# Kernel tuning notes

Measured on AMD Instinct MI355X. Metric: run time of the kernel, lower is better.

## Reference

```python
import jax, jax.numpy as jnp
import numpy as np

H, KVH, DH = 16, 4, 64
DIM = 1024
SCALE_BASE = 4096  # context_len
EPS = 1e-6


def rmsnorm(x, g):
    return x * jax.lax.rsqrt(jnp.mean(x * x, axis=-1, keepdims=True) + EPS) * g


def rope_tables(n, dh, dtype):
    inv_freq = 1.0 / (10000.0 ** (jnp.arange(0, dh, 2, dtype=jnp.float32) / dh))
    t = jnp.arange(n, dtype=jnp.float32) * (SCALE_BASE / n)
    freqs = t[:, None] * inv_freq[None, :]          # [n, dh/2]
    emb = jnp.concatenate([freqs, freqs], axis=-1)  # [n, dh]
    return jnp.cos(emb).astype(dtype), jnp.sin(emb).astype(dtype)


def apply_rope(x, cos, sin):
    # x: [b, h, n, dh]; cos/sin: [n, dh]
    x1, x2 = jnp.split(x, 2, axis=-1)
    rot = jnp.concatenate([-x2, x1], axis=-1)
    return x * cos + rot * sin


def setup_inputs() -> dict:
    key = jax.random.key(0)
    ks = jax.random.split(key, 12)
    B, N = 1, 2048
    std = 0.02
    inp = {
        "x": jax.random.normal(ks[0], (B, N, DIM), jnp.float32),
        "a": jax.random.normal(ks[1], (B, N, DIM), jnp.float32),
        "g_x": jnp.ones((DIM,), jnp.float32),
        "g_a": jnp.ones((DIM,), jnp.float32),
        "Wq_x": jax.random.normal(ks[2], (DIM, H * DH), jnp.float32) * std,
        "Wkv_x": jax.random.normal(ks[3], (DIM, 2 * KVH * DH), jnp.float32) * std,
        "Wq_a": jax.random.normal(ks[4], (DIM, H * DH), jnp.float32) * std,
        "Wkv_a": jax.random.normal(ks[5], (DIM, 2 * KVH * DH), jnp.float32) * std,
        "Wout_x": jax.random.normal(ks[6], (H * DH, DIM), jnp.float32) * std,
        "bout_x": jnp.zeros((DIM,), jnp.float32),
        "Wout_a": jax.random.normal(ks[7], (H * DH, DIM), jnp.float32) * std,
        "bout_a": jnp.zeros((DIM,), jnp.float32),
    }
    return inp


def _split_heads(t, h):
    b, n, hd = t.shape
    return t.reshape(b, n, h, hd // h).transpose(0, 2, 1, 3)  # b h n d


def _stream_qkv(s, g, Wq, Wkv):
    s = rmsnorm(s, g)
    q = _split_heads(s @ Wq, H)                 # [b, H, n, DH]
    kv = s @ Wkv
    k, v = jnp.split(kv, 2, axis=-1)
    k = _split_heads(k, KVH)                    # [b, KVH, n, DH]
    v = _split_heads(v, KVH)
    return q, k, v


def reference(x, a, g_x, g_a, Wq_x, Wkv_x, Wq_a, Wkv_a, Wout_x, bout_x, Wout_a, bout_a):
    B, Nx, _ = x.shape
    Na = a.shape[1]
    scale = DH ** -0.5
    r = H // KVH

    q_x, k_x, v_x = _stream_qkv(x, g_x, Wq_x, Wkv_x)
    q_a, k_a, v_a = _stream_qkv(a, g_a, Wq_a, Wkv_a)

    cos_x, sin_x = rope_tables(Nx, DH, x.dtype)
    cos_a, sin_a = rope_tables(Na, DH, a.dtype)
    q_x, k_x = apply_rope(q_x, cos_x, sin_x), apply_rope(k_x, cos_x, sin_x)
    q_a, k_a = apply_rope(q_a, cos_a, sin_a), apply_rope(k_a, cos_a, sin_a)

    # NOTE: original scales q by dim_head**-0.5 AND sdpa scales again -> 1/DH total
    q_x = q_x * scale
    q_a = q_a * scale

    # GQA expansion: einops 'b h n d -> b (r h) n d' == tile heads
    tile = lambda t: jnp.tile(t, (1, r, 1, 1))
    k_x, v_x, k_a, v_a = tile(k_x), tile(v_x), tile(k_a), tile(v_a)

    # pack [a, x] along seq
    q = jnp.concatenate([q_a, q_x], axis=2)
    k = jnp.concatenate([k_a, k_x], axis=2)
    v = jnp.concatenate([v_a, v_x], axis=2)

    scores = jnp.einsum('bhqd,bhkd->bhqk', q, k) * scale  # sdpa's own scale
    attn = jax.nn.softmax(scores, axis=-1)
    out = jnp.einsum('bhqk,bhkd->bhqd', attn, v)          # [b, H, Na+Nx, DH]

    out_a, out_x = out[:, :, :Na], out[:, :, Na:]
    merge = lambda t: t.transpose(0, 2, 1, 3).reshape(B, -1, H * DH)
    out_x = merge(out_x) @ Wout_x + bout_x
    out_a = merge(out_a) @ Wout_a + bout_a
    return out_x, out_a
```

## Files before the change

### kernel.cpp

```cpp
#include <hip/hip_runtime.h>
#include <hip/hip_bf16.h>
#include <stdint.h>
#include <math.h>


#define NSEQ 2048
#define NJ   4096
#define DIMM 1024
#define LPAD 72

typedef __attribute__((ext_vector_type(4))) float f32x4;
typedef __attribute__((ext_vector_type(8))) short bf16x8;
typedef __attribute__((ext_vector_type(4))) short bf16x4;

__device__ __forceinline__ unsigned short f2bf(float f) {
  union { float f; uint32_t u; } v; v.f = f;
  return (unsigned short)((v.u + 0x7FFFu + ((v.u >> 16) & 1u)) >> 16);
}

__device__ __forceinline__ uint32_t pack2bf(float a, float b) {
  __hip_bfloat162 h = __float22bfloat162_rn(float2{a, b});
  union { __hip_bfloat162 h; uint32_t u; } c; c.h = h;
  return c.u;
}

#if defined(__has_builtin)
#if __has_builtin(__builtin_amdgcn_exp2f)
#define FAST_EXP2(x) __builtin_amdgcn_exp2f(x)
#endif
#endif
#ifndef FAST_EXP2
#define FAST_EXP2(x) exp2f(x)
#endif

__device__ __forceinline__ void glds16(const void* g, void* l) {
  __builtin_amdgcn_global_load_lds(
      (const __attribute__((address_space(1))) unsigned int*)g,
      (__attribute__((address_space(3))) unsigned int*)l, 16, 0, 0);
}

__global__ __launch_bounds__(256) void prep_kernel(
    const float* __restrict__ xa, const float* __restrict__ xx,
    const float* __restrict__ ga, const float* __restrict__ gx,
    const float* __restrict__ wqa, const float* __restrict__ wqx,
    const float* __restrict__ wkva, const float* __restrict__ wkvx,
    const float* __restrict__ woa, const float* __restrict__ wox,
    unsigned short* __restrict__ XN, unsigned short* __restrict__ WQT,
    unsigned short* __restrict__ WKVT, unsigned short* __restrict__ WOT,
    float* __restrict__ cosT, float* __restrict__ sinT) {
  __shared__ float tile[32][33];
  __shared__ float red[4];
  int bid = blockIdx.x, t = threadIdx.x;
  if (bid < 256) {
    int idx = bid * 256 + t;
    int pos = idx >> 5, i = idx & 31;
    double inv = pow(10000.0, -(double)i / 32.0);
    double ang = (double)(2 * pos) * inv;
    cosT[idx] = (float)cos(ang);
    sinT[idx] = (float)sin(ang);
  } else if (bid < 6400) {
    int b = bid - 256;
    int z = b >> 10, yx = b & 1023;
    int n0 = (yx >> 5) * 32, k0 = (yx & 31) * 32;
    int s = z & 1, ty = z >> 1;
    int N = (ty == 1) ? 512 : 1024;
    if (n0 >= N) return;
    const float* src = (z == 0) ? wqa : (z == 1) ? wqx : (z == 2) ? wkva
                     : (z == 3) ? wkvx : (z == 4) ? woa : wox;
    unsigned short* dst = (ty == 0) ? WQT + (size_t)s * 1024 * 1024
                        : (ty == 1) ? WKVT + (size_t)s * 512 * 1024
                                    : WOT + (size_t)s * 1024 * 1024;
    int r = t >> 3, c4 = (t & 7) * 4;
    f32x4 v = *(const f32x4*)(src + (size_t)(k0 + r) * N + n0 + c4);
    tile[r][c4 + 0] = v.x; tile[r][c4 + 1] = v.y;
    tile[r][c4 + 2] = v.z; tile[r][c4 + 3] = v.w;
    __syncthreads();
    int nn = t >> 3, kk = (t & 7) * 4;
    bf16x4 o;
    o.x = (short)f2bf(tile[kk + 0][nn]);
    o.y = (short)f2bf(tile[kk + 1][nn]);
    o.z = (short)f2bf(tile[kk + 2][nn]);
    o.w = (short)f2bf(tile[kk + 3][nn]);
    *(bf16x4*)(dst + (size_t)(n0 + nn) * 1024 + k0 + kk) = o;
  } else {
    int b = bid - 6400;
    int s = b >> 11, row = b & 2047;
    const float* src = (s == 0 ? xa : xx) + (size_t)row * DIMM;
    const float* g = (s == 0 ? ga : gx);
    f32x4 v = *(const f32x4*)(src + t * 4);
    float ss = v.x * v.x + v.y * v.y + v.z * v.z + v.w * v.w;
#pragma unroll
    for (int o = 32; o > 0; o >>= 1) ss += __shfl_xor(ss, o, 64);
    if ((t & 63) == 0) red[t >> 6] = ss;
    __syncthreads();
    float tot = red[0] + red[1] + red[2] + red[3];
    float rs = rsqrtf(tot * (1.0f / DIMM) + 1e-6f);
    f32x4 gv = *(const f32x4*)(g + t * 4);
    bf16x4 o;
    o.x = (short)f2bf(v.x * rs * gv.x);
    o.y = (short)f2bf(v.y * rs * gv.y);
    o.z = (short)f2bf(v.z * rs * gv.z);
    o.w = (short)f2bf(v.w * rs * gv.w);
    *(bf16x4*)(XN + ((size_t)s * NSEQ + row) * DIMM + t * 4) = o;
  }
}

__device__ __forceinline__ void gemm128_mainloop(
    const unsigned short* __restrict__ Ag, const unsigned short* __restrict__ Bg,
    unsigned short* As, unsigned short* Bs, f32x4 acc[4][4]) {
  int t = threadIdx.x;
  int lane = t & 63, wid = t >> 6;
  int wm = (wid >> 1) * 64, wn = (wid & 1) * 64;
  int l15 = lane & 15, quad = lane >> 4;
  int srow = t >> 2, sko = (t & 3) * 8;
  const unsigned short* ga = Ag + (size_t)srow * 1024 + sko;
  const unsigned short* gb = Bg + (size_t)srow * 1024 + sko;
  unsigned short* la = As + t * 8;
  unsigned short* lb = Bs + t * 8;
#pragma unroll
  for (int mi = 0; mi < 4; ++mi)
#pragma unroll
    for (int j = 0; j < 4; ++j) acc[mi][j] = (f32x4){0.f, 0.f, 0.f, 0.f};
  for (int kt = 0; kt < 32; ++kt) {
    int k0 = kt * 32;
    __syncthreads();
    glds16(ga + k0, la);
    glds16(ga + 64 * 1024 + k0, la + 2048);
    glds16(gb + k0, lb);
    glds16(gb + 64 * 1024 + k0, lb + 2048);
    __syncthreads();
    bf16x8 af[4], bfr[4];
#pragma unroll
    for (int mi = 0; mi < 4; ++mi)
      af[mi] = *(const bf16x8*)(As + (wm + mi * 16 + l15) * 32 + quad * 8);
#pragma unroll
    for (int j = 0; j < 4; ++j)
      bfr[j] = *(const bf16x8*)(Bs + (wn + j * 16 + l15) * 32 + quad * 8);
#pragma unroll
    for (int mi = 0; mi < 4; ++mi)
#pragma unroll
      for (int j = 0; j < 4; ++j)
        acc[mi][j] = __builtin_amdgcn_mfma_f32_16x16x32_bf16(af[mi], bfr[j],
                                                             acc[mi][j], 0, 0, 0);
  }
}

__global__ __launch_bounds__(256) void gemm_qkv_kernel(
    const unsigned short* __restrict__ XN, const unsigned short* __restrict__ WQT,
    const unsigned short* __restrict__ WKVT, const float* __restrict__ cosT,
    const float* __restrict__ sinT, unsigned short* __restrict__ QB,
    unsigned short* __restrict__ KB, unsigned short* __restrict__ VT) {
  __shared__ unsigned short As[128 * 32], Bs[128 * 32];
  int n0 = blockIdx.x * 128, m0 = blockIdx.y * 128;
  int s = (m0 >= 2048) ? 1 : 0;
  const unsigned short* Ag = XN + (size_t)m0 * 1024;
  const unsigned short* Bg = (n0 < 1024)
      ? WQT + (size_t)s * 1024 * 1024 + (size_t)n0 * 1024
      : WKVT + (size_t)s * 512 * 1024 + (size_t)(n0 - 1024) * 1024;
  f32x4 acc[4][4];
  gemm128_mainloop(Ag, Bg, As, Bs, acc);
  int t = threadIdx.x, lane = t & 63, wid = t >> 6;
  int wm = (wid >> 1) * 64, wn = (wid & 1) * 64;
  int l15 = lane & 15, quad = lane >> 4;
  int coln = n0 + wn;
  if (coln < 1280) {
    bool isq = coln < 1024;
    float sc = isq ? (1.4426950408889634f / 64.0f) : 1.0f;
    unsigned short* dstBase;
    if (isq) dstBase = QB + (size_t)(coln >> 6) * NJ * 64;
    else     dstBase = KB + (size_t)((coln - 1024) >> 6) * NJ * 64;
#pragma unroll
    for (int mi = 0; mi < 4; ++mi)
#pragma unroll
      for (int r = 0; r < 4; ++r) {
        int jr = m0 + wm + mi * 16 + quad * 4 + r;
        int pos = jr & 2047;
#pragma unroll
        for (int jp = 0; jp < 2; ++jp) {
          int i = jp * 16 + l15;
          float c = cosT[pos * 32 + i], sn = sinT[pos * 32 + i];
          float x1 = acc[mi][jp][r], x2 = acc[mi][jp + 2][r];
          dstBase[(size_t)jr * 64 + jp * 16 + l15]      = f2bf((x1 * c - x2 * sn) * sc);
          dstBase[(size_t)jr * 64 + 32 + jp * 16 + l15] = f2bf((x2 * c + x1 * sn) * sc);
        }
      }
  } else {
    int cvb = coln - 1280;
#pragma unroll
    for (int mi = 0; mi < 4; ++mi)
#pragma unroll
      for (int j = 0; j < 4; ++j) {
        int d = cvb + j * 16 + l15;
        int jr0 = m0 + wm + mi * 16 + quad * 4;
        union { bf16x4 v; uint32_t u[2]; } pv;
        pv.u[0] = pack2bf(acc[mi][j][0], acc[mi][j][1]);
        pv.u[1] = pack2bf(acc[mi][j][2], acc[mi][j][3]);
        *(bf16x4*)(VT + (size_t)d * NJ + jr0) = pv.v;
      }
  }
}

__global__ __launch_bounds__(256, 2) void attn_kernel(
    const unsigned short* __restrict__ QB, const unsigned short* __restrict__ KB,
    const unsigned short* __restrict__ VT, unsigned short* __restrict__ AT) {
  __shared__ __align__(16) unsigned short Ks[2][64 * LPAD];
  __shared__ __align__(16) unsigned short Vs[2][64 * LPAD];
  int h = blockIdx.y, qt = blockIdx.x;
  int hk = h & 3;
  int t = threadIdx.x, lane = t & 63, w = t >> 6;
  int l15 = lane & 15, quad = lane >> 4;
  int qsel = w >> 1, ksel = w & 1;
  int q0 = qt * 128 + qsel * 64;
  bf16x8 qf[4][2];
#pragma unroll
  for (int mi = 0; mi < 4; ++mi) {
    const unsigned short* qp = QB + ((size_t)h * NJ + q0 + mi * 16 + l15) * 64;
    qf[mi][0] = *(const bf16x8*)(qp + quad * 8);
    qf[mi][1] = *(const bf16x8*)(qp + 32 + quad * 8);
  }
  f32x4 oT[4][4];
  f32x4 oL[4];
#pragma unroll
  for (int mi = 0; mi < 4; ++mi) {
    oL[mi] = (f32x4){0.f, 0.f, 0.f, 0.f};
#pragma unroll
    for (int db = 0; db < 4; ++db) oT[mi][db] = (f32x4){0.f, 0.f, 0.f, 0.f};
  }
  bf16x8 vone;
  {
    short one = (l15 == 0) ? (short)0x3F80 : (short)0;
    vone = (bf16x8){one, one, one, one, one, one, one, one};
  }
  const unsigned short* Kg = KB + (size_t)hk * NJ * 64;
  const unsigned short* Vg = VT + (size_t)hk * 64 * NJ;
  int ky = t >> 3, dof = (t & 7) * 8;
  int pky = (ky & 0x23) | ((ky & 0x18) >> 1) | ((ky & 0x04) << 2);
  const unsigned short* KgA = Kg + (size_t)ky * 64 + dof;
  const unsigned short* KgB = Kg + (size_t)(32 + ky) * 64 + dof;
  const unsigned short* VgA = Vg + (size_t)ky * NJ + dof;
  const unsigned short* VgB = Vg + (size_t)(32 + ky) * NJ + dof;
  bf16x8 kr0 = *(const bf16x8*)(KgA);
  bf16x8 kr1 = *(const bf16x8*)(KgB);
  bf16x8 vr0 = *(const bf16x8*)(VgA);
  bf16x8 vr1 = *(const bf16x8*)(VgB);
  *(bf16x8*)(Ks[0] + pky * LPAD + dof) = kr0;
  *(bf16x8*)(Ks[0] + (32 + pky) * LPAD + dof) = kr1;
  *(bf16x8*)(Vs[0] + ky * LPAD + dof) = vr0;
  *(bf16x8*)(Vs[0] + (32 + ky) * LPAD + dof) = vr1;
  kr0 = *(const bf16x8*)(KgA + 4096);
  kr1 = *(const bf16x8*)(KgB + 4096);
  vr0 = *(const bf16x8*)(VgA + 64);
  vr1 = *(const bf16x8*)(VgB + 64);
  __syncthreads();
  for (int kt = 0; kt < 64; ++kt) {
    int cur = kt & 1;
    unsigned short* Kd = Ks[cur ^ 1];
    unsigned short* Vd = Vs[cur ^ 1];
    *(bf16x8*)(Kd + pky * LPAD + dof) = kr0;
    *(bf16x8*)(Kd + (32 + pky) * LPAD + dof) = kr1;
    *(bf16x8*)(Vd + ky * LPAD + dof) = vr0;
    *(bf16x8*)(Vd + (32 + ky) * LPAD + dof) = vr1;
    int tn = (kt + 2) & 63;
    kr0 = *(const bf16x8*)(KgA + (size_t)tn * 4096);
    kr1 = *(const bf16x8*)(KgB + (size_t)tn * 4096);
    vr0 = *(const bf16x8*)(VgA + tn * 64);
    vr1 = *(const bf16x8*)(VgB + tn * 64);
    const unsigned short* Kc = Ks[cur];
    const unsigned short* Vc = Vs[cur];
    f32x4 sx[4][2];
#pragma unroll
    for (int jj = 0; jj < 2; ++jj) {
      int jb = 2 * ksel + jj;
      const unsigned short* kp = Kc + (jb * 16 + l15) * LPAD;
      bf16x8 kf0 = *(const bf16x8*)(kp + quad * 8);
      bf16x8 kf1 = *(const bf16x8*)(kp + 32 + quad * 8);
#pragma unroll
      for (int mi = 0; mi < 4; ++mi) {
        f32x4 z = (f32x4){0.f, 0.f, 0.f, 0.f};
        z = __builtin_amdgcn_mfma_f32_16x16x32_bf16(kf0, qf[mi][0], z, 0, 0, 0);
        z = __builtin_amdgcn_mfma_f32_16x16x32_bf16(kf1, qf[mi][1], z, 0, 0, 0);
        sx[mi][jj] = z;
      }
    }
    bf16x8 pb[4];
#pragma unroll
    for (int mi = 0; mi < 4; ++mi) {
      union { bf16x8 v; uint32_t u[4]; } pk;
      pk.u[0] = pack2bf(FAST_EXP2(sx[mi][0][0]), FAST_EXP2(sx[mi][0][1]));
      pk.u[1] = pack2bf(FAST_EXP2(sx[mi][0][2]), FAST_EXP2(sx[mi][0][3]));
      pk.u[2] = pack2bf(FAST_EXP2(sx[mi][1][0]), FAST_EXP2(sx[mi][1][1]));
      pk.u[3] = pack2bf(FAST_EXP2(sx[mi][1][2]), FAST_EXP2(sx[mi][1][3]));
      pb[mi] = pk.v;
    }
#pragma unroll
    for (int db = 0; db < 4; ++db) {
      bf16x8 va = *(const bf16x8*)(Vc + (db * 16 + l15) * LPAD + ksel * 32 + quad * 8);
#pragma unroll
      for (int mi = 0; mi < 4; ++mi)
        oT[mi][db] = __builtin_amdgcn_mfma_f32_16x16x32_bf16(va, pb[mi],
                                                             oT[mi][db], 0, 0, 0);
    }
#pragma unroll
    for (int mi = 0; mi < 4; ++mi)
      oL[mi] = __builtin_amdgcn_mfma_f32_16x16x32_bf16(vone, pb[mi],
                                                       oL[mi], 0, 0, 0);
    __syncthreads();
  }
  float ls[4];
#pragma unroll
  for (int mi = 0; mi < 4; ++mi) {
    float s = oL[mi][0];
    s += __shfl_xor(s, 16, 64);
    s += __shfl_xor(s, 32, 64);
    ls[mi] = s;
  }
  float* xb = (float*)(qsel == 0 ? &Ks[0][0] : &Vs[0][0]);
  if (ksel == 1) {
    f32x4* dst = (f32x4*)xb + (size_t)lane * 16;
#pragma unroll
    for (int mi = 0; mi < 4; ++mi)
#pragma unroll
      for (int db = 0; db < 4; ++db) dst[mi * 4 + db] = oT[mi][db];
    float* dl = xb + 64 * 64 + lane * 4;
#pragma unroll
    for (int mi = 0; mi < 4; ++mi) dl[mi] = ls[mi];
  }
  __syncthreads();
  if (ksel == 0) {
    const f32x4* src = (const f32x4*)xb + (size_t)lane * 16;
    const float* sl = xb + 64 * 64 + lane * 4;
#pragma unroll
    for (int mi = 0; mi < 4; ++mi) {
      float inv = 1.0f / (ls[mi] + sl[mi]);
      int qrow = q0 + mi * 16 + l15;
#pragma unroll
      for (int db = 0; db < 4; ++db) {
        f32x4 o = oT[mi][db] + src[mi * 4 + db];
        union { bf16x4 v; uint32_t u[2]; } ov;
        ov.u[0] = pack2bf(o[0] * inv, o[1] * inv);
        ov.u[1] = pack2bf(o[2] * inv, o[3] * inv);
        *(bf16x4*)(AT + (size_t)qrow * DIMM + h * 64 + db * 16 + quad * 4) = ov.v;
      }
    }
  }
}

__global__ __launch_bounds__(256) void gemm_out_kernel(
    const unsigned short* __restrict__ AT, const unsigned short* __restrict__ WOT,
    const float* __restrict__ ba, const float* __restrict__ bx,
    float* __restrict__ out) {
  __shared__ unsigned short As[128 * 32], Bs[128 * 32];
  int n0 = blockIdx.x * 128, m0 = blockIdx.y * 128;
  int s = (m0 >= 2048) ? 1 : 0;
  const unsigned short* Ag = AT + (size_t)m0 * 1024;
  const unsigned short* Bg = WOT + (size_t)s * 1024 * 1024 + (size_t)n0 * 1024;
  f32x4 acc[4][4];
  gemm128_mainloop(Ag, Bg, As, Bs, acc);
  int t = threadIdx.x, lane = t & 63, wid = t >> 6;
  int wm = (wid >> 1) * 64, wn = (wid & 1) * 64;
  int l15 = lane & 15, quad = lane >> 4;
  const float* bias = s ? bx : ba;
  float* obase = s ? (out + (size_t)(m0 - 2048) * 1024)
                   : (out + (size_t)2048 * 1024 + (size_t)m0 * 1024);
#pragma unroll
  for (int mi = 0; mi < 4; ++mi)
#pragma unroll
    for (int r = 0; r < 4; ++r) {
      int row = wm + mi * 16 + quad * 4 + r;
#pragma unroll
      for (int j = 0; j < 4; ++j) {
        int col = n0 + wn + j * 16 + l15;
        obase[(size_t)row * 1024 + col] = acc[mi][j][r] + bias[col];
      }
    }
}

extern "C" void kernel_launch(void* const* d_in, const int* in_sizes, int n_in,
                              void* d_out, int out_size, void* d_ws, size_t ws_size,
                              hipStream_t stream) {
  const float* x      = (const float*)d_in[0];
  const float* a      = (const float*)d_in[1];
  const float* g_x    = (const float*)d_in[2];
  const float* g_a    = (const float*)d_in[3];
  const float* Wq_x   = (const float*)d_in[4];
  const float* Wkv_x  = (const float*)d_in[5];
  const float* Wq_a   = (const float*)d_in[6];
  const float* Wkv_a  = (const float*)d_in[7];
  const float* Wout_x = (const float*)d_in[8];
  const float* bout_x = (const float*)d_in[9];
  const float* Wout_a = (const float*)d_in[10];
  const float* bout_a = (const float*)d_in[11];
  float* out = (float*)d_out;

  char* ws = (char*)d_ws;
  const size_t MB = 1024 * 1024;
  unsigned short* XN   = (unsigned short*)(ws);
  unsigned short* WQT  = (unsigned short*)(ws + 8 * MB);
  unsigned short* WKVT = (unsigned short*)(ws + 12 * MB);
  unsigned short* WOT  = (unsigned short*)(ws + 14 * MB);
  unsigned short* QB   = (unsigned short*)(ws + 18 * MB);
  unsigned short* KB   = (unsigned short*)(ws + 26 * MB);
  unsigned short* VT   = (unsigned short*)(ws + 28 * MB);
  float* cosT          = (float*)(ws + 30 * MB);
  float* sinT          = (float*)(ws + 30 * MB + 262144);
  unsigned short* AT   = XN;

  prep_kernel<<<dim3(10496), dim3(256), 0, stream>>>(
      a, x, g_a, g_x, Wq_a, Wq_x, Wkv_a, Wkv_x, Wout_a, Wout_x,
      XN, WQT, WKVT, WOT, cosT, sinT);
  gemm_qkv_kernel<<<dim3(12, 32), dim3(256), 0, stream>>>(
      XN, WQT, WKVT, cosT, sinT, QB, KB, VT);
  attn_kernel<<<dim3(32, 16), dim3(256), 0, stream>>>(QB, KB, VT, AT);
  gemm_out_kernel<<<dim3(8, 32), dim3(256), 0, stream>>>(
      AT, WOT, bout_a, bout_x, out);
}
```

Measured before the change: 225.0 us.

## Load K/V fragments directly from global into registers, removing LDS staging

The attention loop no longer stages K and V tiles through double-buffered shared memory with per-iteration barriers. Each wave now loads its MFMA operand fragments straight from global/L2 into registers, using a two-deep register double buffer and a row permutation that stands in for the old LDS swizzle. This removes the LDS writes and reads and the __syncthreads in the inner loop. In exchange, each wave fetches its own copy of K/V, so global/L2 traffic and register pressure rise, and the loads are less coalesced.

```diff
diff --git a/kernel.cpp b/kernel.cpp
--- a/kernel.cpp
+++ b/kernel.cpp
@@ -7,7 +7,6 @@
 #define NSEQ 2048
 #define NJ   4096
 #define DIMM 1024
-#define LPAD 72
 
 typedef __attribute__((ext_vector_type(4))) float f32x4;
 typedef __attribute__((ext_vector_type(8))) short bf16x8;
@@ -203,8 +202,7 @@
 __global__ __launch_bounds__(256, 2) void attn_kernel(
     const unsigned short* __restrict__ QB, const unsigned short* __restrict__ KB,
     const unsigned short* __restrict__ VT, unsigned short* __restrict__ AT) {
-  __shared__ __align__(16) unsigned short Ks[2][64 * LPAD];
-  __shared__ __align__(16) unsigned short Vs[2][64 * LPAD];
+  __shared__ __align__(16) float comb[2][64 * 68];
   int h = blockIdx.y, qt = blockIdx.x;
   int hk = h & 3;
   int t = threadIdx.x, lane = t & 63, w = t >> 6;
@@ -233,79 +231,74 @@
   }
   const unsigned short* Kg = KB + (size_t)hk * NJ * 64;
   const unsigned short* Vg = VT + (size_t)hk * 64 * NJ;
-  int ky = t >> 3, dof = (t & 7) * 8;
-  int pky = (ky & 0x23) | ((ky & 0x18) >> 1) | ((ky & 0x04) << 2);
-  const unsigned short* KgA = Kg + (size_t)ky * 64 + dof;
-  const unsigned short* KgB = Kg + (size_t)(32 + ky) * 64 + dof;
-  const unsigned short* VgA = Vg + (size_t)ky * NJ + dof;
-  const unsigned short* VgB = Vg + (size_t)(32 + ky) * NJ + dof;
-  bf16x8 kr0 = *(const bf16x8*)(KgA);
-  bf16x8 kr1 = *(const bf16x8*)(KgB);
-  bf16x8 vr0 = *(const bf16x8*)(VgA);
-  bf16x8 vr1 = *(const bf16x8*)(VgB);
-  *(bf16x8*)(Ks[0] + pky * LPAD + dof) = kr0;
-  *(bf16x8*)(Ks[0] + (32 + pky) * LPAD + dof) = kr1;
-  *(bf16x8*)(Vs[0] + ky * LPAD + dof) = vr0;
-  *(bf16x8*)(Vs[0] + (32 + ky) * LPAD + dof) = vr1;
-  kr0 = *(const bf16x8*)(KgA + 4096);
-  kr1 = *(const bf16x8*)(KgB + 4096);
-  vr0 = *(const bf16x8*)(VgA + 64);
-  vr1 = *(const bf16x8*)(VgB + 64);
-  __syncthreads();
-  for (int kt = 0; kt < 64; ++kt) {
-    int cur = kt & 1;
-    unsigned short* Kd = Ks[cur ^ 1];
-    unsigned short* Vd = Vs[cur ^ 1];
-    *(bf16x8*)(Kd + pky * LPAD + dof) = kr0;
-    *(bf16x8*)(Kd + (32 + pky) * LPAD + dof) = kr1;
-    *(bf16x8*)(Vd + ky * LPAD + dof) = vr0;
-    *(bf16x8*)(Vd + (32 + ky) * LPAD + dof) = vr1;
-    int tn = (kt + 2) & 63;
-    kr0 = *(const bf16x8*)(KgA + (size_t)tn * 4096);
-    kr1 = *(const bf16x8*)(KgB + (size_t)tn * 4096);
-    vr0 = *(const bf16x8*)(VgA + tn * 64);
-    vr1 = *(const bf16x8*)(VgB + tn * 64);
-    const unsigned short* Kc = Ks[cur];
-    const unsigned short* Vc = Vs[cur];
-    f32x4 sx[4][2];
-#pragma unroll
-    for (int jj = 0; jj < 2; ++jj) {
-      int jb = 2 * ksel + jj;
-      const unsigned short* kp = Kc + (jb * 16 + l15) * LPAD;
-      bf16x8 kf0 = *(const bf16x8*)(kp + quad * 8);
-      bf16x8 kf1 = *(const bf16x8*)(kp + 32 + quad * 8);
-#pragma unroll
-      for (int mi = 0; mi < 4; ++mi) {
-        f32x4 z = (f32x4){0.f, 0.f, 0.f, 0.f};
-        z = __builtin_amdgcn_mfma_f32_16x16x32_bf16(kf0, qf[mi][0], z, 0, 0, 0);
-        z = __builtin_amdgcn_mfma_f32_16x16x32_bf16(kf1, qf[mi][1], z, 0, 0, 0);
-        sx[mi][jj] = z;
-      }
-    }
-    bf16x8 pb[4];
-#pragma unroll
-    for (int mi = 0; mi < 4; ++mi) {
-      union { bf16x8 v; uint32_t u[4]; } pk;
-      pk.u[0] = pack2bf(FAST_EXP2(sx[mi][0][0]), FAST_EXP2(sx[mi][0][1]));
-      pk.u[1] = pack2bf(FAST_EXP2(sx[mi][0][2]), FAST_EXP2(sx[mi][0][3]));
-      pk.u[2] = pack2bf(FAST_EXP2(sx[mi][1][0]), FAST_EXP2(sx[mi][1][1]));
-      pk.u[3] = pack2bf(FAST_EXP2(sx[mi][1][2]), FAST_EXP2(sx[mi][1][3]));
-      pb[mi] = pk.v;
-    }
-#pragma unroll
-    for (int db = 0; db < 4; ++db) {
-      bf16x8 va = *(const bf16x8*)(Vc + (db * 16 + l15) * LPAD + ksel * 32 + quad * 8);
-#pragma unroll
-      for (int mi = 0; mi < 4; ++mi)
-        oT[mi][db] = __builtin_amdgcn_mfma_f32_16x16x32_bf16(va, pb[mi],
-                                                             oT[mi][db], 0, 0, 0);
-    }
-#pragma unroll
-    for (int mi = 0; mi < 4; ++mi)
-      oL[mi] = __builtin_amdgcn_mfma_f32_16x16x32_bf16(vone, pb[mi],
-                                                       oL[mi], 0, 0, 0);
-    __syncthreads();
-  }
+  int g0 = 32 * ksel + 8 * (l15 >> 2) + (l15 & 3);
+  const unsigned short* kp0 = Kg + (size_t)g0 * 64 + quad * 8;
+  const unsigned short* kp1 = Kg + (size_t)(g0 + 4) * 64 + quad * 8;
+  const unsigned short* vp0 = Vg + (size_t)(0 * 16 + l15) * NJ + ksel * 32 + quad * 8;
+  const unsigned short* vp1 = Vg + (size_t)(1 * 16 + l15) * NJ + ksel * 32 + quad * 8;
+  const unsigned short* vp2 = Vg + (size_t)(2 * 16 + l15) * NJ + ksel * 32 + quad * 8;
+  const unsigned short* vp3 = Vg + (size_t)(3 * 16 + l15) * NJ + ksel * 32 + quad * 8;
+
+  struct KV { bf16x8 k00, k01, k10, k11, v0, v1, v2, v3; };
+
+#define LOADKV(F, KT) do {                                               \
+    size_t ko_ = (size_t)(KT) * 4096;                                    \
+    int vo_ = (KT) * 64;                                                 \
+    (F).k00 = *(const bf16x8*)(kp0 + ko_);                               \
+    (F).k01 = *(const bf16x8*)(kp0 + ko_ + 32);                          \
+    (F).k10 = *(const bf16x8*)(kp1 + ko_);                               \
+    (F).k11 = *(const bf16x8*)(kp1 + ko_ + 32);                          \
+    (F).v0  = *(const bf16x8*)(vp0 + vo_);                               \
+    (F).v1  = *(const bf16x8*)(vp1 + vo_);                               \
+    (F).v2  = *(const bf16x8*)(vp2 + vo_);                               \
+    (F).v3  = *(const bf16x8*)(vp3 + vo_);                               \
+  } while (0)
+
+#define COMPUTE(F) do {                                                  \
+    f32x4 sx_[4][2];                                                     \
+    _Pragma("unroll")                                                    \
+    for (int mi = 0; mi < 4; ++mi) {                                     \
+      f32x4 z0 = (f32x4){0.f, 0.f, 0.f, 0.f};                            \
+      z0 = __builtin_amdgcn_mfma_f32_16x16x32_bf16((F).k00, qf[mi][0], z0, 0, 0, 0); \
+      z0 = __builtin_amdgcn_mfma_f32_16x16x32_bf16((F).k01, qf[mi][1], z0, 0, 0, 0); \
+      sx_[mi][0] = z0;                                                   \
+      f32x4 z1 = (f32x4){0.f, 0.f, 0.f, 0.f};                            \
+      z1 = __builtin_amdgcn_mfma_f32_16x16x32_bf16((F).k10, qf[mi][0], z1, 0, 0, 0); \
+      z1 = __builtin_amdgcn_mfma_f32_16x16x32_bf16((F).k11, qf[mi][1], z1, 0, 0, 0); \
+      sx_[mi][1] = z1;                                                   \
+    }                                                                    \
+    bf16x8 pb_[4];                                                       \
+    _Pragma("unroll")                                                    \
+    for (int mi = 0; mi < 4; ++mi) {                                     \
+      union { bf16x8 v; uint32_t u[4]; } pk_;                            \
+      pk_.u[0] = pack2bf(FAST_EXP2(sx_[mi][0][0]), FAST_EXP2(sx_[mi][0][1])); \
+      pk_.u[1] = pack2bf(FAST_EXP2(sx_[mi][0][2]), FAST_EXP2(sx_[mi][0][3])); \
+      pk_.u[2] = pack2bf(FAST_EXP2(sx_[mi][1][0]), FAST_EXP2(sx_[mi][1][1])); \
+      pk_.u[3] = pack2bf(FAST_EXP2(sx_[mi][1][2]), FAST_EXP2(sx_[mi][1][3])); \
+      pb_[mi] = pk_.v;                                                   \
+    }                                                                    \
+    _Pragma("unroll")                                                    \
+    for (int mi = 0; mi < 4; ++mi) {                                     \
+      oT[mi][0] = __builtin_amdgcn_mfma_f32_16x16x32_bf16((F).v0, pb_[mi], oT[mi][0], 0, 0, 0); \
+      oT[mi][1] = __builtin_amdgcn_mfma_f32_16x16x32_bf16((F).v1, pb_[mi], oT[mi][1], 0, 0, 0); \
+      oT[mi][2] = __builtin_amdgcn_mfma_f32_16x16x32_bf16((F).v2, pb_[mi], oT[mi][2], 0, 0, 0); \
+      oT[mi][3] = __builtin_amdgcn_mfma_f32_16x16x32_bf16((F).v3, pb_[mi], oT[mi][3], 0, 0, 0); \
+      oL[mi] = __builtin_amdgcn_mfma_f32_16x16x32_bf16(vone, pb_[mi], oL[mi], 0, 0, 0); \
+    }                                                                    \
+  } while (0)
+
+  KV fA, fB;
+  LOADKV(fA, 0);
+  LOADKV(fB, 1);
+  for (int kt = 0; kt < 64; kt += 2) {
+    COMPUTE(fA);
+    LOADKV(fA, (kt + 2) & 63);
+    COMPUTE(fB);
+    LOADKV(fB, (kt + 3) & 63);
+  }
+#undef LOADKV
+#undef COMPUTE
+
   float ls[4];
 #pragma unroll
   for (int mi = 0; mi < 4; ++mi) {
@@ -314,7 +307,7 @@
     s += __shfl_xor(s, 32, 64);
     ls[mi] = s;
   }
-  float* xb = (float*)(qsel == 0 ? &Ks[0][0] : &Vs[0][0]);
+  float* xb = comb[qsel];
   if (ksel == 1) {
     f32x4* dst = (f32x4*)xb + (size_t)lane * 16;
 #pragma unroll
```

New measurement: 270.9 us. +20.4%, slower.
